# Kernel optimization log

Hardware: AMD Instinct MI355X
Metric: run time of the kernel (lower is better)

## Reference

```python
import jax, jax.numpy as jnp
import numpy as np

B, S, D, H = 2, 2048, 1024, 16
DQ = D // H
EPS = 1e-5


def setup_inputs() -> dict:
    key = jax.random.key(0)
    ks = jax.random.split(key, 6)
    scale = 0.02
    return {
        "x": jax.random.normal(ks[0], (B, S, D), dtype=jnp.float32),
        "ln_g": jnp.ones((D,), dtype=jnp.float32),
        "ln_b": jnp.zeros((D,), dtype=jnp.float32),
        "Wq": jax.random.normal(ks[1], (D, D), dtype=jnp.float32) * scale,
        "bq": jnp.zeros((D,), dtype=jnp.float32),
        "Wk": jax.random.normal(ks[2], (D, D), dtype=jnp.float32) * scale,
        "bk": jnp.zeros((D,), dtype=jnp.float32),
        "Wv": jax.random.normal(ks[3], (D, D), dtype=jnp.float32) * scale,
        "bv": jnp.zeros((D,), dtype=jnp.float32),
        "Wo": jax.random.normal(ks[4], (D, D), dtype=jnp.float32) * scale,
        "bo": jnp.zeros((D,), dtype=jnp.float32),
    }


def reference(x, ln_g, ln_b, Wq, bq, Wk, bk, Wv, bv, Wo, bo):
    # pre-LayerNorm (torch default eps=1e-5, biased variance)
    mu = jnp.mean(x, axis=-1, keepdims=True)
    var = jnp.mean((x - mu) ** 2, axis=-1, keepdims=True)
    xn = (x - mu) * jax.lax.rsqrt(var + EPS) * ln_g + ln_b

    # QKV projections; weights stored [d_in, d_out]
    q = xn @ Wq + bq  # [B,S,D]
    k = xn @ Wk + bk
    v = xn @ Wv + bv

    # split heads -> [B,H,S,DQ]
    def heads(t):
        return t.reshape(B, S, H, DQ).transpose(0, 2, 1, 3)
    q, k, v = heads(q), heads(k), heads(v)

    scores = jnp.einsum("bhqd,bhkd->bhqk", q, k) / jnp.sqrt(jnp.float32(DQ))
    causal = jnp.tril(jnp.ones((S, S), dtype=bool))  # True = keep
    scores = jnp.where(causal, scores, -jnp.inf)
    probs = jax.nn.softmax(scores, axis=-1)
    attn = jnp.einsum("bhqk,bhkd->bhqd", probs, v)  # [B,H,S,DQ]

    # merge heads: [B,H,S,DQ] -> [B,S,H*DQ] (matches transpose/flatten/transpose)
    merged = attn.transpose(0, 2, 1, 3).reshape(B, S, D)
    out = merged @ Wo + bo
    return out + x
```

## Files before the change

### kernel.cpp

```cpp
#include <hip/hip_runtime.h>
#include <math.h>

#define BB 2
#define SS 2048
#define DD 1024
#define HH 16
#define DQK 64
#define NROWS (BB * SS)
#define NE ((size_t)BB * SS * DD)

using short8 = __attribute__((ext_vector_type(8))) short;
using f32x4  = __attribute__((ext_vector_type(4))) float;

__device__ __forceinline__ ushort f2bf(float f) {
  union { float f; unsigned u; } c; c.f = f;
  return (ushort)((c.u + 0x7fffu + ((c.u >> 16) & 1u)) >> 16);
}

__device__ __forceinline__ unsigned cvt_pk_bf16(float lo, float hi) {
  unsigned r;
  asm("v_cvt_pk_bf16_f32 %0, %1, %2" : "=v"(r) : "v"(lo), "v"(hi));
  return r;
}

__device__ __forceinline__ f32x4 mfma16(short8 a, short8 b, f32x4 c) {
  return __builtin_amdgcn_mfma_f32_16x16x32_bf16(a, b, c, 0, 0, 0);
}

typedef __attribute__((address_space(1))) const unsigned gas_u32;
typedef __attribute__((address_space(3))) unsigned las_u32;
__device__ __forceinline__ void gload_lds16(const void* g, void* l) {
  __builtin_amdgcn_global_load_lds((gas_u32*)g, (las_u32*)l, 16, 0, 0);
}

__global__ __launch_bounds__(256) void prep(const float* __restrict__ x,
                                            const float* __restrict__ g,
                                            const float* __restrict__ bta,
                                            ushort* __restrict__ xn,
                                            const float* __restrict__ Wq,
                                            const float* __restrict__ Wk,
                                            const float* __restrict__ Wv,
                                            const float* __restrict__ Wo,
                                            ushort* __restrict__ wt) {
  __shared__ float tile[64][65];
  const int t = threadIdx.x;
  if (blockIdx.x < NROWS) {
    const int row = blockIdx.x;
    float4 v = ((const float4*)(x + (size_t)row * DD))[t];
    float s  = v.x + v.y + v.z + v.w;
    float ss = v.x * v.x + v.y * v.y + v.z * v.z + v.w * v.w;
#pragma unroll
    for (int off = 32; off > 0; off >>= 1) {
      s  += __shfl_xor(s, off);
      ss += __shfl_xor(ss, off);
    }
    const int wid = t >> 6, lane = t & 63;
    if (lane == 0) { tile[0][wid] = s; tile[0][4 + wid] = ss; }
    __syncthreads();
    const float stot  = tile[0][0] + tile[0][1] + tile[0][2] + tile[0][3];
    const float sstot = tile[0][4] + tile[0][5] + tile[0][6] + tile[0][7];
    const float mu  = stot * (1.0f / DD);
    const float var = sstot * (1.0f / DD) - mu * mu;
    const float inv = rsqrtf(var + 1e-5f);
    const float4 g4 = ((const float4*)g)[t];
    const float4 b4 = ((const float4*)bta)[t];
    ushort4 o;
    o.x = f2bf((v.x - mu) * inv * g4.x + b4.x);
    o.y = f2bf((v.y - mu) * inv * g4.y + b4.y);
    o.z = f2bf((v.z - mu) * inv * g4.z + b4.z);
    o.w = f2bf((v.w - mu) * inv * g4.w + b4.w);
    ((ushort4*)(xn + (size_t)row * DD))[t] = o;
  } else {
    const int wb = blockIdx.x - NROWS;
    const int z = wb >> 8;
    const int k0 = (wb & 15) * 64, n0 = ((wb >> 4) & 15) * 64;
    const float* W = (z == 0) ? Wq : (z == 1) ? Wk : (z == 2) ? Wv : Wo;
    ushort* dst = wt + (size_t)z * DD * DD;
    const int tr = t >> 4, tc = (t & 15) * 4;
#pragma unroll
    for (int rr = 0; rr < 64; rr += 16) {
      float4 v = *(const float4*)(W + (size_t)(k0 + rr + tr) * DD + n0 + tc);
      tile[rr + tr][tc + 0] = v.x;
      tile[rr + tr][tc + 1] = v.y;
      tile[rr + tr][tc + 2] = v.z;
      tile[rr + tr][tc + 3] = v.w;
    }
    __syncthreads();
#pragma unroll
    for (int rr = 0; rr < 64; rr += 16) {
      const int n = rr + tr;
      ushort4 o;
      o.x = f2bf(tile[tc + 0][n]);
      o.y = f2bf(tile[tc + 1][n]);
      o.z = f2bf(tile[tc + 2][n]);
      o.w = f2bf(tile[tc + 3][n]);
      *(ushort4*)(dst + (size_t)(n0 + n) * DD + k0 + tc) = o;
    }
  }
}

#define GEMM_CORE(Ag, Bg)                                                     \
  f32x4 acc[4][4];                                                            \
  _Pragma("unroll")                                                           \
  for (int m = 0; m < 4; ++m)                                                 \
    _Pragma("unroll")                                                         \
    for (int n = 0; n < 4; ++n) acc[m][n] = (f32x4){0.f, 0.f, 0.f, 0.f};     \
  const int cs = ((t & 3) * 16) ^ (((t >> 3) & 3) * 16);                      \
  const int fsw = ((r16 >> 1) & 3) * 16;                                      \
  {                                                                           \
    GSTAGE(Ag, Bg, 0, 0);                                                     \
    GSTAGE(Ag, Bg, 1, 32);                                                    \
    int cb = 0;                                                               \
    for (int k0 = 0; k0 < DD; k0 += 32) {                                     \
      __builtin_amdgcn_sched_barrier(0);                                      \
      if (k0 + 32 < DD) {                                                     \
        asm volatile("s_waitcnt vmcnt(4)" ::: "memory");                      \
      } else {                                                                \
        asm volatile("s_waitcnt vmcnt(0)" ::: "memory");                      \
      }                                                                       \
      __builtin_amdgcn_s_barrier();                                           \
      __builtin_amdgcn_sched_barrier(0);                                      \
      if (k0 + 64 < DD) {                                                     \
        int nb = cb + 2; if (nb >= 3) nb -= 3;                                \
        GSTAGE(Ag, Bg, nb, k0 + 64);                                          \
      }                                                                       \
      const char* Ac = (const char*)&As[cb][0][0];                            \
      const char* Bc = (const char*)&Bs[cb][0][0];                            \
      short8 af[4], bf[4];                                                    \
      _Pragma("unroll")                                                       \
      for (int m = 0; m < 4; ++m)                                             \
        af[m] = *(const short8*)(Ac + (wr * 64 + m * 16 + r16) * 64 +         \
                                 ((g * 16) ^ fsw));                           \
      _Pragma("unroll")                                                       \
      for (int n = 0; n < 4; ++n)                                             \
        bf[n] = *(const short8*)(Bc + (wc * 64 + n * 16 + r16) * 64 +         \
                                 ((g * 16) ^ fsw));                           \
      _Pragma("unroll")                                                       \
      for (int m = 0; m < 4; ++m)                                             \
        _Pragma("unroll")                                                     \
        for (int n = 0; n < 4; ++n) acc[m][n] = mfma16(af[m], bf[n], acc[m][n]); \
      cb = (cb + 1 == 3) ? 0 : cb + 1;                                        \
    }                                                                         \
  }

#define GSTAGE(Ag, Bg, buf, k0)                                               \
  {                                                                           \
    _Pragma("unroll")                                                         \
    for (int i = 0; i < 2; ++i) {                                             \
      gload_lds16(Ag + (size_t)(row0 + i * 64 + (t >> 2)) * (DD * 2) +        \
                      (k0) * 2 + cs,                                          \
                  (char*)&As[buf][0][0] + i * 4096 + t * 16);                 \
      gload_lds16(Bg + (size_t)(col0 + i * 64 + (t >> 2)) * (DD * 2) +        \
                      (k0) * 2 + cs,                                          \
                  (char*)&Bs[buf][0][0] + i * 4096 + t * 16);                 \
    }                                                                         \
  }

#define GEMM_CORE_O(Ag, Bg)                                                   \
  f32x4 acc[4][2];                                                            \
  _Pragma("unroll")                                                           \
  for (int m = 0; m < 4; ++m)                                                 \
    _Pragma("unroll")                                                         \
    for (int n = 0; n < 2; ++n) acc[m][n] = (f32x4){0.f, 0.f, 0.f, 0.f};     \
  const int cs = ((t & 3) * 16) ^ (((t >> 3) & 3) * 16);                      \
  const int fsw = ((r16 >> 1) & 3) * 16;                                      \
  {                                                                           \
    GSTAGE_O(Ag, Bg, 0, 0);                                                   \
    GSTAGE_O(Ag, Bg, 1, 32);                                                  \
    int cb = 0;                                                               \
    for (int k0 = 0; k0 < DD; k0 += 32) {                                     \
      __builtin_amdgcn_sched_barrier(0);                                      \
      if (k0 + 32 < DD) {                                                     \
        asm volatile("s_waitcnt vmcnt(3)" ::: "memory");                      \
      } else {                                                                \
        asm volatile("s_waitcnt vmcnt(0)" ::: "memory");                      \
      }                                                                       \
      __builtin_amdgcn_s_barrier();                                           \
      __builtin_amdgcn_sched_barrier(0);                                      \
      if (k0 + 64 < DD) {                                                     \
        int nb = cb + 2; if (nb >= 3) nb -= 3;                                \
        GSTAGE_O(Ag, Bg, nb, k0 + 64);                                        \
      }                                                                       \
      const char* Ac = (const char*)&As[cb][0][0];                            \
      const char* Bc = (const char*)&Bs[cb][0][0];                            \
      short8 af[4], bf[2];                                                    \
      _Pragma("unroll")                                                       \
      for (int m = 0; m < 4; ++m)                                             \
        af[m] = *(const short8*)(Ac + (wr * 64 + m * 16 + r16) * 64 +         \
                                 ((g * 16) ^ fsw));                           \
      _Pragma("unroll")                                                       \
      for (int n = 0; n < 2; ++n)                                             \
        bf[n] = *(const short8*)(Bc + (wc * 32 + n * 16 + r16) * 64 +         \
                                 ((g * 16) ^ fsw));                           \
      _Pragma("unroll")                                                       \
      for (int m = 0; m < 4; ++m)                                             \
        _Pragma("unroll")                                                     \
        for (int n = 0; n < 2; ++n) acc[m][n] = mfma16(af[m], bf[n], acc[m][n]); \
      cb = (cb + 1 == 3) ? 0 : cb + 1;                                        \
    }                                                                         \
  }

#define GSTAGE_O(Ag, Bg, buf, k0)                                             \
  {                                                                           \
    _Pragma("unroll")                                                         \
    for (int i = 0; i < 2; ++i)                                               \
      gload_lds16(Ag + (size_t)(row0 + i * 64 + (t >> 2)) * (DD * 2) +        \
                      (k0) * 2 + cs,                                          \
                  (char*)&As[buf][0][0] + i * 4096 + t * 16);                 \
    gload_lds16(Bg + (size_t)(col0 + (t >> 2)) * (DD * 2) + (k0) * 2 + cs,    \
                (char*)&Bs[buf][0][0] + t * 16);                              \
  }

__global__ __launch_bounds__(256) void gemm_qkv(
    const ushort* __restrict__ A, const ushort* __restrict__ wt,
    const float* __restrict__ bq, const float* __restrict__ bk,
    const float* __restrict__ bv, ushort* __restrict__ qb,
    ushort* __restrict__ kb, ushort* __restrict__ vt) {
  __shared__ ushort As[3][128][32];
  __shared__ ushort Bs[3][128][32];
  const int t = threadIdx.x;
  const int lane = t & 63;
  const int w = t >> 6, wr = w >> 1, wc = w & 1;
  const int r16 = lane & 15, g = lane >> 4;
  const int row0 = blockIdx.x * 128;
  const int mat = blockIdx.y >> 3;
  const int col0 = (blockIdx.y & 7) * 128;
  const char* Ag = (const char*)A;
  const char* Bg = (const char*)(wt + (size_t)mat * DD * DD);
  const float* bias = (mat == 0) ? bq : (mat == 1) ? bk : bv;
  const float scl = (mat == 0) ? 0.125f * 1.44269504f : 1.0f;

  GEMM_CORE(Ag, Bg)

#pragma unroll
  for (int n = 0; n < 4; ++n) {
    const int c = col0 + wc * 64 + n * 16 + r16;
    const float bc = bias[c];
#pragma unroll
    for (int m = 0; m < 4; ++m) {
      const int rbase = row0 + wr * 64 + m * 16 + g * 4;
      if (mat < 2) {
        ushort* outb = (mat == 0) ? qb : kb;
#pragma unroll
        for (int e = 0; e < 4; ++e)
          outb[(size_t)(rbase + e) * DD + c] = f2bf((acc[m][n][e] + bc) * scl);
      } else {
        uint2 st;
        st.x = cvt_pk_bf16(acc[m][n][0] + bc, acc[m][n][1] + bc);
        st.y = cvt_pk_bf16(acc[m][n][2] + bc, acc[m][n][3] + bc);
        const size_t vrow = (size_t)((rbase >> 11) * HH + (c >> 6)) * DQK + (c & 63);
        *(uint2*)(vt + vrow * SS + (rbase & 2047)) = st;
      }
    }
  }
}

__global__ __launch_bounds__(256) void gemm_o(
    const ushort* __restrict__ A, const ushort* __restrict__ Bt,
    const float* __restrict__ bias, const float* __restrict__ resid,
    float* __restrict__ outf) {
  __shared__ ushort As[3][128][32];
  __shared__ ushort Bs[3][64][32];
  const int t = threadIdx.x;
  const int lane = t & 63;
  const int w = t >> 6, wr = w >> 1, wc = w & 1;
  const int r16 = lane & 15, g = lane >> 4;
  const int row0 = blockIdx.x * 128;
  const int col0 = blockIdx.y * 64;
  const char* Ag = (const char*)A;
  const char* Bg = (const char*)Bt;

  GEMM_CORE_O(Ag, Bg)

#pragma unroll
  for (int n = 0; n < 2; ++n) {
    const int c = col0 + wc * 32 + n * 16 + r16;
    const float bc = bias[c];
#pragma unroll
    for (int m = 0; m < 4; ++m) {
      const int rbase = row0 + wr * 64 + m * 16 + g * 4;
#pragma unroll
      for (int e = 0; e < 4; ++e) {
        const size_t idx = (size_t)(rbase + e) * DD + c;
        outf[idx] = acc[m][n][e] + bc + resid[idx];
      }
    }
  }
}

__global__ __launch_bounds__(256) void attn_mfma(const ushort* __restrict__ Q,
                                                 const ushort* __restrict__ K,
                                                 const ushort* __restrict__ Vt,
                                                 ushort* __restrict__ O) {
  __shared__ ushort Ks[3][64][64];
  __shared__ ushort Vs[3][64][64];

  const int t = threadIdx.x, lane = t & 63, ww = t >> 6;
  const int r16 = lane & 15, g = lane >> 4;

  const int bid = blockIdx.x;
  const int xcd = bid & 7;
  const int bh = xcd * 4 + ((bid >> 3) & 3);
  const int p = bid >> 5;
  const int nt1 = 32 - p;
  const int nt2 = p + 1;
  const int b = bh >> 4, h = bh & 15;
  const size_t tokbase = (size_t)b * SS;
  const size_t hoff = (size_t)h * DQK;

  const int srow = t >> 3;
  const int scol = (t & 7) * 16;
  const char* Kb = (const char*)(K + tokbase * DD + hoff);
  const char* Vb = (const char*)(Vt + (size_t)bh * DQK * SS);
  const int sw = ((r16 & 3) | ((r16 >> 1) & 4)) << 4;
  const int rlo = (r16 & 3) + ((r16 >> 2) << 3);

#define STAGE(buf, j0)                                                        \
  {                                                                           \
    _Pragma("unroll")                                                         \
    for (int i = 0; i < 2; ++i) {                                             \
      const int R = i * 32 + srow;                                            \
      const int Cs = scol ^ (((R & 3) | ((R >> 1) & 4)) << 4);                \
      gload_lds16(Kb + ((size_t)((j0) + R) * DD) * 2 + Cs,                    \
                  (char*)&Ks[buf][0][0] + i * 4096 + ww * 1024);              \
    }                                                                         \
    _Pragma("unroll")                                                         \
    for (int i = 0; i < 2; ++i) {                                             \
      const int R = i * 32 + srow;                                            \
      const int Cs = scol ^ (((R & 3) | ((R >> 1) & 4)) << 4);                \
      gload_lds16(Vb + ((size_t)R * SS + (j0)) * 2 + Cs,                      \
                  (char*)&Vs[buf][0][0] + i * 4096 + ww * 1024);              \
    }                                                                         \
  }

  int q0 = (31 - p) * 64 + ww * 16;
  const int q02 = p * 64 + ww * 16;
  short8 qc0, qc1, q2f0, q2f1;
  qc0 = *(const short8*)(Q + (tokbase + q0 + r16) * DD + hoff + 0 * 32 + g * 8);
  qc1 = *(const short8*)(Q + (tokbase + q0 + r16) * DD + hoff + 1 * 32 + g * 8);
  q2f0 = *(const short8*)(Q + (tokbase + q02 + r16) * DD + hoff + 0 * 32 + g * 8);
  q2f1 = *(const short8*)(Q + (tokbase + q02 + r16) * DD + hoff + 1 * 32 + g * 8);

  f32x4 o[4];
#pragma unroll
  for (int dt = 0; dt < 4; ++dt) o[dt] = (f32x4){0.f, 0.f, 0.f, 0.f};
  float rm = -INFINITY, rl = 0.f;

  STAGE(0, 0);
  STAGE(1, 64);
  int cb = 0;
#pragma unroll 1
  for (int vt = 0; vt < 33; ++vt) {
    if (vt == nt1) {
      float rls = rl;
      rls += __shfl_xor(rls, 16);
      rls += __shfl_xor(rls, 32);
      const float inv = 1.0f / rls;
#pragma unroll
      for (int dt = 0; dt < 4; ++dt) {
        uint2 st;
        st.x = cvt_pk_bf16(o[dt][0] * inv, o[dt][1] * inv);
        st.y = cvt_pk_bf16(o[dt][2] * inv, o[dt][3] * inv);
        *(uint2*)(O + (tokbase + q0 + r16) * DD + hoff + dt * 16 + g * 4) = st;
        o[dt] = (f32x4){0.f, 0.f, 0.f, 0.f};
      }
      rm = -INFINITY; rl = 0.f;
      q0 = q02; qc0 = q2f0; qc1 = q2f1;
    }

    __builtin_amdgcn_sched_barrier(0);
    asm volatile("s_waitcnt vmcnt(6)" ::: "memory");
    __builtin_amdgcn_s_barrier();
    __builtin_amdgcn_sched_barrier(0);

    {
      const int w2 = vt + 2;
      int jj = (w2 < nt1) ? w2 : (w2 - nt1);
      if (w2 >= nt1 && jj >= nt2) jj = 0;
      int nb = cb + 2; if (nb >= 3) nb -= 3;
      STAGE(nb, jj * 64);
    }

    const char* Kc = (const char*)&Ks[cb][0][0];
    const char* Vc = (const char*)&Vs[cb][0][0];

    f32x4 s4[4];
    __builtin_amdgcn_s_setprio(1);
#pragma unroll
    for (int t2 = 0; t2 < 4; ++t2) {
      const int kk = rlo + (t2 & 1) * 4 + (t2 >> 1) * 32;
      const int sk = ((kk & 3) | ((kk >> 1) & 4)) << 4;
      const int rb = kk * 128;
      const short8 k0 = *(const short8*)(Kc + rb + ((g * 16) ^ sk));
      const short8 k1 = *(const short8*)(Kc + rb + ((64 + g * 16) ^ sk));
      f32x4 s = mfma16(k0, qc0, (f32x4){0.f, 0.f, 0.f, 0.f});
      s4[t2] = mfma16(k1, qc1, s);
    }
    __builtin_amdgcn_s_setprio(0);

    const bool lastseg = (vt == nt1 - 1) || (vt == 32);
    if (lastseg) {
      const int tloc = (vt >= nt1) ? (vt - nt1) : vt;
      const int thrl = q0 + r16 - g * 8 - tloc * 64;
#pragma unroll
      for (int t2 = 0; t2 < 4; ++t2) {
        const int bb = (t2 & 1) * 4 + (t2 >> 1) * 32;
#pragma unroll
        for (int r = 0; r < 4; ++r)
          s4[t2][r] = (bb + r <= thrl) ? s4[t2][r] : -INFINITY;
      }
    }

    float mx = fmaxf(
        fmaxf(fmaxf(fmaxf(s4[0][0], s4[0][1]), fmaxf(s4[0][2], s4[0][3])),
              fmaxf(fmaxf(s4[1][0], s4[1][1]), fmaxf(s4[1][2], s4[1][3]))),
        fmaxf(fmaxf(fmaxf(s4[2][0], s4[2][1]), fmaxf(s4[2][2], s4[2][3])),
              fmaxf(fmaxf(s4[3][0], s4[3][1]), fmaxf(s4[3][2], s4[3][3]))));

    if (!__all(mx - rm <= 8.f)) {
      float mf = fmaxf(mx, __shfl_xor(mx, 16));
      mf = fmaxf(mf, __shfl_xor(mf, 32));
      const float mn = fmaxf(rm, mf);
      const float sc = __builtin_amdgcn_exp2f(rm - mn);
      rl *= sc;
#pragma unroll
      for (int dt = 0; dt < 4; ++dt) o[dt] *= sc;
      rm = mn;
    }

    union { unsigned u[4]; short8 s; } pbu[2];
#pragma unroll
    for (int t2 = 0; t2 < 4; ++t2) {
      const float p0 = __builtin_amdgcn_exp2f(s4[t2][0] - rm);
      const float p1 = __builtin_amdgcn_exp2f(s4[t2][1] - rm);
      const float p2 = __builtin_amdgcn_exp2f(s4[t2][2] - rm);
      const float p3 = __builtin_amdgcn_exp2f(s4[t2][3] - rm);
      rl += (p0 + p1) + (p2 + p3);
      pbu[t2 >> 1].u[(t2 & 1) * 2 + 0] = cvt_pk_bf16(p0, p1);
      pbu[t2 >> 1].u[(t2 & 1) * 2 + 1] = cvt_pk_bf16(p2, p3);
    }

    __builtin_amdgcn_sched_barrier(0);
    asm volatile("s_waitcnt vmcnt(8)" ::: "memory");
    __builtin_amdgcn_s_barrier();
    __builtin_amdgcn_sched_barrier(0);

    __builtin_amdgcn_s_setprio(1);
#pragma unroll
    for (int kc = 0; kc < 2; ++kc) {
#pragma unroll
      for (int dt = 0; dt < 4; ++dt) {
        const short8 vf = *(const short8*)(Vc + (dt * 16 + r16) * 128 +
                                           ((kc * 64 + g * 16) ^ sw));
        o[dt] = mfma16(vf, pbu[kc].s, o[dt]);
      }
    }
    __builtin_amdgcn_s_setprio(0);
    cb = (cb + 1 == 3) ? 0 : cb + 1;
  }
#undef STAGE

  rl += __shfl_xor(rl, 16);
  rl += __shfl_xor(rl, 32);
  const float inv = 1.0f / rl;
#pragma unroll
  for (int dt = 0; dt < 4; ++dt) {
    uint2 st;
    st.x = cvt_pk_bf16(o[dt][0] * inv, o[dt][1] * inv);
    st.y = cvt_pk_bf16(o[dt][2] * inv, o[dt][3] * inv);
    *(uint2*)(O + (tokbase + q0 + r16) * DD + hoff + dt * 16 + g * 4) = st;
  }
}

extern "C" void kernel_launch(void* const* d_in, const int* in_sizes, int n_in,
                              void* d_out, int out_size, void* d_ws, size_t ws_size,
                              hipStream_t stream) {
  const float* x    = (const float*)d_in[0];
  const float* ln_g = (const float*)d_in[1];
  const float* ln_b = (const float*)d_in[2];
  const float* Wq   = (const float*)d_in[3];
  const float* bq   = (const float*)d_in[4];
  const float* Wk   = (const float*)d_in[5];
  const float* bk   = (const float*)d_in[6];
  const float* Wv   = (const float*)d_in[7];
  const float* bv   = (const float*)d_in[8];
  const float* Wo   = (const float*)d_in[9];
  const float* bo   = (const float*)d_in[10];
  float* out = (float*)d_out;

  ushort* ws  = (ushort*)d_ws;
  ushort* xn  = ws;
  ushort* qb  = xn + NE;
  ushort* kb  = qb + NE;
  ushort* vt  = kb + NE;
  ushort* ab  = vt + NE;
  ushort* wt  = ab + NE;
  ushort* wot = wt + (size_t)3 * DD * DD;

  prep<<<NROWS + 1024, 256, 0, stream>>>(x, ln_g, ln_b, xn, Wq, Wk, Wv, Wo, wt);

  gemm_qkv<<<dim3(NROWS / 128, 24), 256, 0, stream>>>(xn, wt, bq, bk, bv,
                                                      qb, kb, vt);

  attn_mfma<<<BB * HH * (SS / 128), 256, 0, stream>>>(qb, kb, vt, ab);

  gemm_o<<<dim3(NROWS / 128, DD / 64), 256, 0, stream>>>(ab, wot, bo, x, out);
}
```

Measured before the change: 108.6 us.

## Split paired causal query tiles into separate blocks with double-buffered K/V

Each attention block now handles a single 64-row query tile instead of a complementary pair (long plus short), so the grid doubles to 1024 blocks. The heavy tiles are dispatched first via a remapped ordering. The K/V staging goes from a three-buffer ring to a manually unrolled two-buffer ping-pong with precomputed LDS offsets and full vmcnt(0) waits. This is meant to raise occupancy and parallelism and cut per-iteration address math, at the cost of less prefetch depth and load imbalance that now falls to the hardware scheduler.

```diff
diff --git a/kernel.cpp b/kernel.cpp
--- a/kernel.cpp
+++ b/kernel.cpp
@@ -292,8 +292,8 @@
                                                  const ushort* __restrict__ K,
                                                  const ushort* __restrict__ Vt,
                                                  ushort* __restrict__ O) {
-  __shared__ ushort Ks[3][64][64];
-  __shared__ ushort Vs[3][64][64];
+  __shared__ ushort Ks[2][64][64];
+  __shared__ ushort Vs[2][64][64];
 
   const int t = threadIdx.x, lane = t & 63, ww = t >> 6;
   const int r16 = lane & 15, g = lane >> 4;
@@ -301,164 +301,149 @@
   const int bid = blockIdx.x;
   const int xcd = bid & 7;
   const int bh = xcd * 4 + ((bid >> 3) & 3);
-  const int p = bid >> 5;
-  const int nt1 = 32 - p;
-  const int nt2 = p + 1;
+  const int m = (bid >> 5) & 7;
+  const int j = bid >> 8;
+  const int qb = (j == 0) ? (31 - m) : (j == 1) ? m : (j == 2) ? (23 - m) : (8 + m);
   const int b = bh >> 4, h = bh & 15;
   const size_t tokbase = (size_t)b * SS;
   const size_t hoff = (size_t)h * DQK;
+  const int q0 = qb * 64 + ww * 16;
+  const int nt = qb + 1;
 
   const int srow = t >> 3;
   const int scol = (t & 7) * 16;
+  const int Cs = scol ^ (((srow & 3) | ((srow >> 1) & 4)) << 4);
   const char* Kb = (const char*)(K + tokbase * DD + hoff);
   const char* Vb = (const char*)(Vt + (size_t)bh * DQK * SS);
+  const char* kbase0 = Kb + (size_t)srow * (DD * 2) + Cs;
+  const char* kbase1 = Kb + (size_t)(srow + 32) * (DD * 2) + Cs;
+  const char* vbase0 = Vb + (size_t)srow * (SS * 2) + Cs;
+  const char* vbase1 = Vb + (size_t)(srow + 32) * (SS * 2) + Cs;
+  char* ksd = (char*)&Ks[0][0][0] + ww * 1024;
+  char* vsd = (char*)&Vs[0][0][0] + ww * 1024;
+
+#define STAGE(BOFF, TILE)                                                     \
+  {                                                                           \
+    const size_t ko = (size_t)(TILE) << 17;                 \
+    const size_t vo = (size_t)(TILE) << 7;                   \
+    gload_lds16(kbase0 + ko, ksd + (BOFF));                                   \
+    gload_lds16(kbase1 + ko, ksd + (BOFF) + 4096);                            \
+    gload_lds16(vbase0 + vo, vsd + (BOFF));                                   \
+    gload_lds16(vbase1 + vo, vsd + (BOFF) + 4096);                            \
+  }
+
   const int sw = ((r16 & 3) | ((r16 >> 1) & 4)) << 4;
   const int rlo = (r16 & 3) + ((r16 >> 2) << 3);
-
-#define STAGE(buf, j0)                                                        \
-  {                                                                           \
-    _Pragma("unroll")                                                         \
-    for (int i = 0; i < 2; ++i) {                                             \
-      const int R = i * 32 + srow;                                            \
-      const int Cs = scol ^ (((R & 3) | ((R >> 1) & 4)) << 4);                \
-      gload_lds16(Kb + ((size_t)((j0) + R) * DD) * 2 + Cs,                    \
-                  (char*)&Ks[buf][0][0] + i * 4096 + ww * 1024);              \
-    }                                                                         \
-    _Pragma("unroll")                                                         \
-    for (int i = 0; i < 2; ++i) {                                             \
-      const int R = i * 32 + srow;                                            \
-      const int Cs = scol ^ (((R & 3) | ((R >> 1) & 4)) << 4);                \
-      gload_lds16(Vb + ((size_t)R * SS + (j0)) * 2 + Cs,                      \
-                  (char*)&Vs[buf][0][0] + i * 4096 + ww * 1024);              \
-    }                                                                         \
-  }
-
-  int q0 = (31 - p) * 64 + ww * 16;
-  const int q02 = p * 64 + ww * 16;
-  short8 qc0, qc1, q2f0, q2f1;
-  qc0 = *(const short8*)(Q + (tokbase + q0 + r16) * DD + hoff + 0 * 32 + g * 8);
-  qc1 = *(const short8*)(Q + (tokbase + q0 + r16) * DD + hoff + 1 * 32 + g * 8);
-  q2f0 = *(const short8*)(Q + (tokbase + q02 + r16) * DD + hoff + 0 * 32 + g * 8);
-  q2f1 = *(const short8*)(Q + (tokbase + q02 + r16) * DD + hoff + 1 * 32 + g * 8);
+  int offk[4][2], offv[4][2];
+#pragma unroll
+  for (int t2 = 0; t2 < 4; ++t2) {
+    const int kk = rlo + (t2 & 1) * 4 + (t2 >> 1) * 32;
+    const int sk = ((kk & 3) | ((kk >> 1) & 4)) << 4;
+    offk[t2][0] = kk * 128 + ((g * 16) ^ sk);
+    offk[t2][1] = kk * 128 + ((64 + g * 16) ^ sk);
+  }
+#pragma unroll
+  for (int dt = 0; dt < 4; ++dt) {
+    offv[dt][0] = (dt * 16 + r16) * 128 + ((g * 16) ^ sw);
+    offv[dt][1] = (dt * 16 + r16) * 128 + ((64 + g * 16) ^ sw);
+  }
+  const char* KsB = (const char*)&Ks[0][0][0];
+  const char* VsB = (const char*)&Vs[0][0][0];
+
+  const short8 qc0 = *(const short8*)(Q + (tokbase + q0 + r16) * DD + hoff + g * 8);
+  const short8 qc1 = *(const short8*)(Q + (tokbase + q0 + r16) * DD + hoff + 32 + g * 8);
 
   f32x4 o[4];
 #pragma unroll
   for (int dt = 0; dt < 4; ++dt) o[dt] = (f32x4){0.f, 0.f, 0.f, 0.f};
   float rm = -INFINITY, rl = 0.f;
 
+#define COMPUTE(BOFF, DOMASK, TLOC)                                           \
+  {                                                                           \
+    f32x4 s4[4];                                                              \
+    __builtin_amdgcn_s_setprio(1);                                            \
+    _Pragma("unroll")                                                         \
+    for (int t2 = 0; t2 < 4; ++t2) {                                          \
+      const short8 k0 = *(const short8*)(KsB + (BOFF) + offk[t2][0]);         \
+      const short8 k1 = *(const short8*)(KsB + (BOFF) + offk[t2][1]);         \
+      f32x4 s = mfma16(k0, qc0, (f32x4){0.f, 0.f, 0.f, 0.f});                 \
+      s4[t2] = mfma16(k1, qc1, s);                                            \
+    }                                                                         \
+    __builtin_amdgcn_s_setprio(0);                                            \
+    if (DOMASK) {                                                             \
+      const int thrl = q0 + r16 - g * 8 - (TLOC) * 64;                        \
+      _Pragma("unroll")                                                       \
+      for (int t2 = 0; t2 < 4; ++t2) {                                        \
+        const int bb = (t2 & 1) * 4 + (t2 >> 1) * 32;                         \
+        _Pragma("unroll")                                                     \
+        for (int r = 0; r < 4; ++r)                                           \
+          s4[t2][r] = (bb + r <= thrl) ? s4[t2][r] : -INFINITY;               \
+      }                                                                       \
+    }                                                                         \
+    float mx = fmaxf(                                                         \
+        fmaxf(fmaxf(fmaxf(s4[0][0], s4[0][1]), fmaxf(s4[0][2], s4[0][3])),    \
+              fmaxf(fmaxf(s4[1][0], s4[1][1]), fmaxf(s4[1][2], s4[1][3]))),   \
+        fmaxf(fmaxf(fmaxf(s4[2][0], s4[2][1]), fmaxf(s4[2][2], s4[2][3])),    \
+              fmaxf(fmaxf(s4[3][0], s4[3][1]), fmaxf(s4[3][2], s4[3][3]))));  \
+    if (!__all(mx - rm <= 8.f)) {                                             \
+      float mf = fmaxf(mx, __shfl_xor(mx, 16));                               \
+      mf = fmaxf(mf, __shfl_xor(mf, 32));                                     \
+      const float mn = fmaxf(rm, mf);                                         \
+      const float sc = __builtin_amdgcn_exp2f(rm - mn);                       \
+      rl *= sc;                                                               \
+      _Pragma("unroll")                                                       \
+      for (int dt = 0; dt < 4; ++dt) o[dt] *= sc;                             \
+      rm = mn;                                                                \
+    }                                                                         \
+    union { unsigned u[4]; short8 s; } pbu[2];                                \
+    _Pragma("unroll")                                                         \
+    for (int t2 = 0; t2 < 4; ++t2) {                                          \
+      const float p0 = __builtin_amdgcn_exp2f(s4[t2][0] - rm);                \
+      const float p1 = __builtin_amdgcn_exp2f(s4[t2][1] - rm);                \
+      const float p2 = __builtin_amdgcn_exp2f(s4[t2][2] - rm);                \
+      const float p3 = __builtin_amdgcn_exp2f(s4[t2][3] - rm);                \
+      rl += (p0 + p1) + (p2 + p3);                                            \
+      pbu[t2 >> 1].u[(t2 & 1) * 2 + 0] = cvt_pk_bf16(p0, p1);                 \
+      pbu[t2 >> 1].u[(t2 & 1) * 2 + 1] = cvt_pk_bf16(p2, p3);                 \
+    }                                                                         \
+    __builtin_amdgcn_s_setprio(1);                                            \
+    _Pragma("unroll")                                                         \
+    for (int kc = 0; kc < 2; ++kc)                                            \
+      _Pragma("unroll")                                                       \
+      for (int dt = 0; dt < 4; ++dt) {                                        \
+        const short8 vf = *(const short8*)(VsB + (BOFF) + offv[dt][kc]);      \
+        o[dt] = mfma16(vf, pbu[kc].s, o[dt]);                                 \
+      }                                                                       \
+    __builtin_amdgcn_s_setprio(0);                                            \
+  }
+
+#define WAITBAR                                                               \
+  __builtin_amdgcn_sched_barrier(0);                                          \
+  asm volatile("s_waitcnt vmcnt(0)" ::: "memory");                            \
+  __builtin_amdgcn_s_barrier();                                               \
+  __builtin_amdgcn_sched_barrier(0);
+
   STAGE(0, 0);
-  STAGE(1, 64);
-  int cb = 0;
+  int tt = 0;
 #pragma unroll 1
-  for (int vt = 0; vt < 33; ++vt) {
-    if (vt == nt1) {
-      float rls = rl;
-      rls += __shfl_xor(rls, 16);
-      rls += __shfl_xor(rls, 32);
-      const float inv = 1.0f / rls;
-#pragma unroll
-      for (int dt = 0; dt < 4; ++dt) {
-        uint2 st;
-        st.x = cvt_pk_bf16(o[dt][0] * inv, o[dt][1] * inv);
-        st.y = cvt_pk_bf16(o[dt][2] * inv, o[dt][3] * inv);
-        *(uint2*)(O + (tokbase + q0 + r16) * DD + hoff + dt * 16 + g * 4) = st;
-        o[dt] = (f32x4){0.f, 0.f, 0.f, 0.f};
-      }
-      rm = -INFINITY; rl = 0.f;
-      q0 = q02; qc0 = q2f0; qc1 = q2f1;
-    }
-
-    __builtin_amdgcn_sched_barrier(0);
-    asm volatile("s_waitcnt vmcnt(6)" ::: "memory");
-    __builtin_amdgcn_s_barrier();
-    __builtin_amdgcn_sched_barrier(0);
-
+  for (; tt + 2 <= nt; tt += 2) {
+    WAITBAR;
+    STAGE(8192, tt + 1);
+    COMPUTE(0, false, 0);
+    WAITBAR;
     {
-      const int w2 = vt + 2;
-      int jj = (w2 < nt1) ? w2 : (w2 - nt1);
-      if (w2 >= nt1 && jj >= nt2) jj = 0;
-      int nb = cb + 2; if (nb >= 3) nb -= 3;
-      STAGE(nb, jj * 64);
-    }
-
-    const char* Kc = (const char*)&Ks[cb][0][0];
-    const char* Vc = (const char*)&Vs[cb][0][0];
-
-    f32x4 s4[4];
-    __builtin_amdgcn_s_setprio(1);
-#pragma unroll
-    for (int t2 = 0; t2 < 4; ++t2) {
-      const int kk = rlo + (t2 & 1) * 4 + (t2 >> 1) * 32;
-      const int sk = ((kk & 3) | ((kk >> 1) & 4)) << 4;
-      const int rb = kk * 128;
-      const short8 k0 = *(const short8*)(Kc + rb + ((g * 16) ^ sk));
-      const short8 k1 = *(const short8*)(Kc + rb + ((64 + g * 16) ^ sk));
-      f32x4 s = mfma16(k0, qc0, (f32x4){0.f, 0.f, 0.f, 0.f});
-      s4[t2] = mfma16(k1, qc1, s);
-    }
-    __builtin_amdgcn_s_setprio(0);
-
-    const bool lastseg = (vt == nt1 - 1) || (vt == 32);
-    if (lastseg) {
-      const int tloc = (vt >= nt1) ? (vt - nt1) : vt;
-      const int thrl = q0 + r16 - g * 8 - tloc * 64;
-#pragma unroll
-      for (int t2 = 0; t2 < 4; ++t2) {
-        const int bb = (t2 & 1) * 4 + (t2 >> 1) * 32;
-#pragma unroll
-        for (int r = 0; r < 4; ++r)
-          s4[t2][r] = (bb + r <= thrl) ? s4[t2][r] : -INFINITY;
-      }
-    }
-
-    float mx = fmaxf(
-        fmaxf(fmaxf(fmaxf(s4[0][0], s4[0][1]), fmaxf(s4[0][2], s4[0][3])),
-              fmaxf(fmaxf(s4[1][0], s4[1][1]), fmaxf(s4[1][2], s4[1][3]))),
-        fmaxf(fmaxf(fmaxf(s4[2][0], s4[2][1]), fmaxf(s4[2][2], s4[2][3])),
-              fmaxf(fmaxf(s4[3][0], s4[3][1]), fmaxf(s4[3][2], s4[3][3]))));
-
-    if (!__all(mx - rm <= 8.f)) {
-      float mf = fmaxf(mx, __shfl_xor(mx, 16));
-      mf = fmaxf(mf, __shfl_xor(mf, 32));
-      const float mn = fmaxf(rm, mf);
-      const float sc = __builtin_amdgcn_exp2f(rm - mn);
-      rl *= sc;
-#pragma unroll
-      for (int dt = 0; dt < 4; ++dt) o[dt] *= sc;
-      rm = mn;
-    }
-
-    union { unsigned u[4]; short8 s; } pbu[2];
-#pragma unroll
-    for (int t2 = 0; t2 < 4; ++t2) {
-      const float p0 = __builtin_amdgcn_exp2f(s4[t2][0] - rm);
-      const float p1 = __builtin_amdgcn_exp2f(s4[t2][1] - rm);
-      const float p2 = __builtin_amdgcn_exp2f(s4[t2][2] - rm);
-      const float p3 = __builtin_amdgcn_exp2f(s4[t2][3] - rm);
-      rl += (p0 + p1) + (p2 + p3);
-      pbu[t2 >> 1].u[(t2 & 1) * 2 + 0] = cvt_pk_bf16(p0, p1);
-      pbu[t2 >> 1].u[(t2 & 1) * 2 + 1] = cvt_pk_bf16(p2, p3);
-    }
-
-    __builtin_amdgcn_sched_barrier(0);
-    asm volatile("s_waitcnt vmcnt(8)" ::: "memory");
-    __builtin_amdgcn_s_barrier();
-    __builtin_amdgcn_sched_barrier(0);
-
-    __builtin_amdgcn_s_setprio(1);
-#pragma unroll
-    for (int kc = 0; kc < 2; ++kc) {
-#pragma unroll
-      for (int dt = 0; dt < 4; ++dt) {
-        const short8 vf = *(const short8*)(Vc + (dt * 16 + r16) * 128 +
-                                           ((kc * 64 + g * 16) ^ sw));
-        o[dt] = mfma16(vf, pbu[kc].s, o[dt]);
-      }
-    }
-    __builtin_amdgcn_s_setprio(0);
-    cb = (cb + 1 == 3) ? 0 : cb + 1;
+      int pj = tt + 2; if (pj >= nt) pj = 0;
+      STAGE(0, pj);
+    }
+    COMPUTE(8192, (tt + 2 == nt), (tt + 1));
+  }
+  if (tt < nt) {
+    WAITBAR;
+    COMPUTE(0, true, tt);
   }
 #undef STAGE
+#undef COMPUTE
+#undef WAITBAR
 
   rl += __shfl_xor(rl, 16);
   rl += __shfl_xor(rl, 32);
@@ -502,7 +487,7 @@
   gemm_qkv<<<dim3(NROWS / 128, 24), 256, 0, stream>>>(xn, wt, bq, bk, bv,
                                                       qb, kb, vt);
 
-  attn_mfma<<<BB * HH * (SS / 128), 256, 0, stream>>>(qb, kb, vt, ab);
+  attn_mfma<<<BB * HH * (SS / 64), 256, 0, stream>>>(qb, kb, vt, ab);
 
   gemm_o<<<dim3(NROWS / 128, DD / 64), 256, 0, stream>>>(ab, wot, bo, x, out);
 }
```

Result: faster. 103.6 us (-4.6%).
